# Kernel tuning notes

Measured on AMD Instinct MI355X. Metric: run time of the kernel, lower is better.

## Reference

```python
import jax, jax.numpy as jnp
import numpy as np

V, E, H, B, L = 128, 256, 4, 1024, 64
EPS5, EPS6 = 1e-5, 1e-6


def layer_norm(x, g, b, eps):
    m = x.mean(-1, keepdims=True)
    v = ((x - m) ** 2).mean(-1, keepdims=True)
    return (x - m) * jax.lax.rsqrt(v + eps) * g + b


def get_pos(max_len, emb_dim):
    # matches torch get_pos: freq[i] = 10000**(-i/half)
    half = emb_dim // 2
    freq = jnp.power(10000.0, -jnp.arange(half, dtype=jnp.float32) / half)
    phase = jnp.arange(max_len, dtype=jnp.float32)[:, None] * freq[None, :]
    pe = jnp.zeros((max_len, emb_dim), jnp.float32)
    pe = pe.at[:, 0::2].set(jnp.sin(phase)).at[:, 1::2].set(jnp.cos(phase))
    return pe


def setup_inputs() -> dict:
    key = jax.random.key(0)
    ks = jax.random.split(key, 8)
    char_code = jax.random.randint(ks[0], (B, L), 0, V)
    emb_table = (jax.random.normal(ks[1], (V, E), jnp.float32) * 0.02).at[0].set(0.0)  # padding_idx=0
    qkv_w = jax.random.normal(ks[2], (3 * E * H, E), jnp.float32) * 0.02
    fc_w = jax.random.normal(ks[3], (E, E * H), jnp.float32) * 0.02
    fc_b = jnp.zeros((E,), jnp.float32)
    ff_w1 = jax.random.normal(ks[4], (E, E), jnp.float32) * 0.02
    ff_b1 = jnp.zeros((E,), jnp.float32)
    ff_w2 = jax.random.normal(ks[5], (E, E), jnp.float32) * 0.02
    ff_b2 = jnp.zeros((E,), jnp.float32)
    ones = jnp.ones((E,), jnp.float32)
    zeros = jnp.zeros((E,), jnp.float32)
    return dict(char_code=char_code, max_len=L, emb_table=emb_table, qkv_w=qkv_w,
                ln0_g=ones, ln0_b=zeros, fc_w=fc_w, fc_b=fc_b,
                sln_g=ones, sln_b=zeros, ln1_g=ones, ln1_b=zeros,
                ff_w1=ff_w1, ff_b1=ff_b1, ff_w2=ff_w2, ff_b2=ff_b2,
                ffln_g=ones, ffln_b=zeros, ln2_g=ones, ln2_b=zeros)


def reference(char_code, max_len, emb_table, qkv_w, ln0_g, ln0_b, fc_w, fc_b,
              sln_g, sln_b, ln1_g, ln1_b, ff_w1, ff_b1, ff_w2, ff_b2,
              ffln_g, ffln_b, ln2_g, ln2_b):
    cc = char_code[:, :max_len]                      # [B,L]
    pos = get_pos(max_len, E)                        # [L,E]
    x = layer_norm(emb_table[cc] + pos[None], ln0_g, ln0_b, EPS5)  # [B,L,E]
    mask = (cc == 0)                                 # [B,L] key mask

    # scaled_dot_product_attention (eval mode, dropout inactive)
    x2 = x + pos[None]                               # pos added a second time (faithful)
    qkv = jnp.einsum('ble,fe->blf', x2, qkv_w)       # [B,L,3*E*H]
    qkv = qkv.reshape(B, max_len, H, 3 * E).transpose(0, 2, 1, 3)  # [B,H,L,3E]
    q, k, v = jnp.split(qkv, 3, axis=-1)             # each [B,H,L,E]
    qk = jnp.einsum('bhqe,bhke->bhqk', q, k) / (E ** 0.5)
    qk = jnp.where(mask[:, None, None, :], -jnp.inf, qk)
    attn = jax.nn.softmax(qk, axis=-1)               # [B,H,L,L]
    nm = (~mask).astype(jnp.float32)                 # [B,L]
    nw = nm.sum(-1)                                  # [B]
    score = jnp.einsum('bq,bhqk->bhk', nm, attn) / nw[:, None, None]  # [B,H,L]
    out = jnp.einsum('bhl,bhle->bhe', score, v)      # [B,H,E]
    out = out.reshape(B, H * E) @ fc_w.T + fc_b      # [B,E]
    out = layer_norm(out, sln_g, sln_b, EPS5)

    word = layer_norm(out + x.mean(1), ln1_g, ln1_b, EPS5)
    # FeedForward bug in source: returns layer_norm(x), ignoring x + layers(x)
    ff = layer_norm(word, ffln_g, ffln_b, EPS6)
    word = ff + word
    word = layer_norm(word, ln2_g, ln2_b, EPS5)
    return word
```

## Files before the change

### kernel.cpp

```cpp
#include <hip/hip_runtime.h>


typedef __attribute__((ext_vector_type(8))) short bf16x8;
typedef __attribute__((ext_vector_type(4))) float f32x4;

__device__ __forceinline__ float wred_sum(float v) {
#pragma unroll
  for (int off = 32; off > 0; off >>= 1) v += __shfl_xor(v, off, 64);
  return v;
}
__device__ __forceinline__ float bf2f(unsigned short u) {
  union { unsigned int i; float f; } x; x.i = ((unsigned int)u) << 16; return x.f;
}
__device__ __forceinline__ unsigned short f2bf(float f) {
  union { float f; unsigned int i; } x; x.f = f;
  unsigned int r = x.i + 0x7FFFu + ((x.i >> 16) & 1u);
  return (unsigned short)(r >> 16);
}
__device__ __forceinline__ void gld16(const unsigned short* g, unsigned short* l) {
  __builtin_amdgcn_global_load_lds(
      (const __attribute__((address_space(1))) unsigned int*)g,
      (__attribute__((address_space(3))) unsigned int*)l, 16, 0, 0);
}
__device__ __forceinline__ float fast_freq(float i) {
  return exp2f(i * (-13.287712379549449f / 128.0f));
}

__global__ __launch_bounds__(256) void prep_kernel(const float* qkv_w, const float* fc_w,
                                                   const float* emb, const float* ln0_g,
                                                   const float* ln0_b, float* posmean,
                                                   unsigned short* NTb, unsigned short* wfoldb,
                                                   unsigned short* x2tb) {
  __shared__ float T[64][65];
  __shared__ unsigned short As[64 * 64];
  __shared__ unsigned short Bs[64 * 64];
  int bid = blockIdx.x, t = threadIdx.x;

  if (bid < 128) {
    int w = t >> 6, lane = t & 63;
    int li = lane & 15, hi = lane >> 4;
    int r = t >> 4, c4 = (t & 15) * 4;
    bool isNT = bid < 64;
    int sub = isNT ? bid : bid - 64;
    int h = sub >> 4;
    int tm = (sub >> 2) & 3;
    int tn = sub & 3;
    int m0 = tm * 64, n0 = tn * 64;
    f32x4 acc[4] = {};
    for (int kt = 0; kt < 4; ++kt) {
      int k0 = kt * 64;
      if (isNT) {
        __syncthreads();
#pragma unroll
        for (int rep = 0; rep < 4; ++rep) {
          int il = rep * 16 + r;
          float4 v = *(const float4*)(qkv_w + (size_t)(h * 768 + 256 + k0 + il) * 256 + m0 + c4);
          T[il][c4] = v.x; T[il][c4 + 1] = v.y; T[il][c4 + 2] = v.z; T[il][c4 + 3] = v.w;
        }
        __syncthreads();
#pragma unroll
        for (int rep = 0; rep < 4; ++rep) {
          int el = rep * 16 + r;
          As[el * 64 + c4 + 0] = f2bf(T[c4 + 0][el]);
          As[el * 64 + c4 + 1] = f2bf(T[c4 + 1][el]);
          As[el * 64 + c4 + 2] = f2bf(T[c4 + 2][el]);
          As[el * 64 + c4 + 3] = f2bf(T[c4 + 3][el]);
        }
      } else {
        __syncthreads();
#pragma unroll
        for (int rep = 0; rep < 4; ++rep) {
          int rl = rep * 16 + r;
          float4 v = *(const float4*)(fc_w + (size_t)(m0 + rl) * 1024 + h * 256 + k0 + c4);
          As[rl * 64 + c4 + 0] = f2bf(v.x);
          As[rl * 64 + c4 + 1] = f2bf(v.y);
          As[rl * 64 + c4 + 2] = f2bf(v.z);
          As[rl * 64 + c4 + 3] = f2bf(v.w);
        }
      }
      {
        int sel = isNT ? 0 : 512;
        __syncthreads();
#pragma unroll
        for (int rep = 0; rep < 4; ++rep) {
          int il = rep * 16 + r;
          float4 v = *(const float4*)(qkv_w + (size_t)(h * 768 + sel + k0 + il) * 256 + n0 + c4);
          T[il][c4] = v.x; T[il][c4 + 1] = v.y; T[il][c4 + 2] = v.z; T[il][c4 + 3] = v.w;
        }
        __syncthreads();
#pragma unroll
        for (int rep = 0; rep < 4; ++rep) {
          int el = rep * 16 + r;
          Bs[el * 64 + c4 + 0] = f2bf(T[c4 + 0][el]);
          Bs[el * 64 + c4 + 1] = f2bf(T[c4 + 1][el]);
          Bs[el * 64 + c4 + 2] = f2bf(T[c4 + 2][el]);
          Bs[el * 64 + c4 + 3] = f2bf(T[c4 + 3][el]);
        }
      }
      __syncthreads();
#pragma unroll
      for (int kk = 0; kk < 2; ++kk) {
        bf16x8 bf = *(const bf16x8*)(Bs + (w * 16 + li) * 64 + kk * 32 + hi * 8);
#pragma unroll
        for (int m = 0; m < 4; ++m) {
          bf16x8 af = *(const bf16x8*)(As + (m * 16 + li) * 64 + kk * 32 + hi * 8);
          acc[m] = __builtin_amdgcn_mfma_f32_16x16x32_bf16(af, bf, acc[m], 0, 0, 0);
        }
      }
    }
    if (isNT) {
      unsigned short* C = NTb + (size_t)h * 65536;
      int col = n0 + w * 16 + li;
#pragma unroll
      for (int m = 0; m < 4; ++m)
#pragma unroll
        for (int j = 0; j < 4; ++j)
          C[(size_t)(m0 + m * 16 + hi * 4 + j) * 256 + col] = f2bf(acc[m][j]);
    } else {
      int col = h * 256 + n0 + w * 16 + li;
#pragma unroll
      for (int m = 0; m < 4; ++m)
#pragma unroll
        for (int j = 0; j < 4; ++j)
          wfoldb[(size_t)(m0 + m * 16 + hi * 4 + j) * 1024 + col] = f2bf(acc[m][j]);
    }
  } else if (bid == 128) {
    int e = t;
    float freq = fast_freq((float)(e >> 1));
    float s = 0.f;
    for (int l = 0; l < 64; ++l) {
      float ph = (float)l * freq;
      s += (e & 1) ? __cosf(ph) : __sinf(ph);
    }
    posmean[e] = s * (1.0f / 64.0f);
  } else {
    int w = t >> 6, lane = t & 63;
    int row = (bid - 129) * 4 + w;
    int c = row >> 6, l = row & 63;
    int e0 = lane * 4;
    float fr0 = fast_freq((float)(e0 >> 1));
    float fr1 = fast_freq((float)(e0 >> 1) + 1.0f);
    float p0 = (float)l * fr0, p1 = (float)l * fr1;
    float4 pv = make_float4(__sinf(p0), __cosf(p0), __sinf(p1), __cosf(p1));
    float4 ev = *(const float4*)(emb + c * 256 + e0);
    float v0 = ev.x + pv.x, v1 = ev.y + pv.y, v2 = ev.z + pv.z, v3 = ev.w + pv.w;
    float s = wred_sum(v0 + v1 + v2 + v3);
    float q = wred_sum(v0 * v0 + v1 * v1 + v2 * v2 + v3 * v3);
    float mean = s * (1.0f / 256.0f);
    float var = q * (1.0f / 256.0f) - mean * mean;
    float rstd = rsqrtf(var + 1e-5f);
    float4 gv = *(const float4*)(ln0_g + e0);
    float4 bv = *(const float4*)(ln0_b + e0);
    *(ushort4*)(x2tb + (size_t)row * 256 + e0) = make_ushort4(
        f2bf((v0 - mean) * rstd * gv.x + bv.x + pv.x),
        f2bf((v1 - mean) * rstd * gv.y + bv.y + pv.y),
        f2bf((v2 - mean) * rstd * gv.z + bv.z + pv.z),
        f2bf((v3 - mean) * rstd * gv.w + bv.w + pv.w));
  }
}

__global__ __launch_bounds__(256) void gemm128_kernel(const unsigned short* A,
                                                      const unsigned short* B,
                                                      unsigned short* C) {
  __shared__ unsigned short S[2 * 128 * 64];
  unsigned short* As = S;
  unsigned short* Bs = S + 128 * 64;
  int t = threadIdx.x, w = t >> 6, lane = t & 63;
  int m0 = blockIdx.y * 128, n0 = blockIdx.x * 128, z = blockIdx.z;
  B += (size_t)z * 65536;
  int wr = w >> 1, wc = w & 1;
  f32x4 acc[4][4] = {};
  int r_in = lane >> 3, cb = (lane & 7) * 8;
  for (int kt = 0; kt < 4; ++kt) {
#pragma unroll
    for (int it = 0; it < 4; ++it) {
      int rowblk = it * 32 + w * 8;
      gld16(A + (size_t)(m0 + rowblk + r_in) * 256 + kt * 64 + cb, As + rowblk * 64);
      gld16(B + (size_t)(n0 + rowblk + r_in) * 256 + kt * 64 + cb, Bs + rowblk * 64);
    }
    __syncthreads();
#pragma unroll
    for (int kk = 0; kk < 2; ++kk) {
      bf16x8 af[4], bfr[4];
#pragma unroll
      for (int m = 0; m < 4; ++m)
        af[m] = *(const bf16x8*)(As + (wr * 64 + m * 16 + (lane & 15)) * 64 + kk * 32 + (lane >> 4) * 8);
#pragma unroll
      for (int n = 0; n < 4; ++n)
        bfr[n] = *(const bf16x8*)(Bs + (wc * 64 + n * 16 + (lane & 15)) * 64 + kk * 32 + (lane >> 4) * 8);
#pragma unroll
      for (int m = 0; m < 4; ++m)
#pragma unroll
        for (int n = 0; n < 4; ++n)
          acc[m][n] = __builtin_amdgcn_mfma_f32_16x16x32_bf16(af[m], bfr[n], acc[m][n], 0, 0, 0);
    }
    __syncthreads();
  }
  unsigned short* Cs = S;
#pragma unroll
  for (int m = 0; m < 4; ++m)
#pragma unroll
    for (int n = 0; n < 4; ++n) {
      int row = wr * 64 + m * 16 + ((lane >> 4)) * 4;
      int col = wc * 64 + n * 16 + (lane & 15);
#pragma unroll
      for (int j = 0; j < 4; ++j)
        Cs[(row + j) * 128 + col] = f2bf(acc[m][n][j]);
    }
  __syncthreads();
#pragma unroll
  for (int it = 0; it < 8; ++it) {
    int row = it * 16 + (t >> 4);
    int ce = (t & 15) * 8;
    *(bf16x8*)(C + (size_t)(m0 + row) * 1024 + z * 256 + n0 + ce) =
        *(const bf16x8*)(Cs + row * 128 + ce);
  }
}

__global__ __launch_bounds__(512, 4) void attn_kernel(const int* cc, const unsigned short* yt,
                                                      const unsigned short* x2tb,
                                                      const float* posmean,
                                                      unsigned short* svb, float* xmb) {
  __shared__ unsigned short X2s[4 * 4112];
  __shared__ float s_sp[8][64];
  __shared__ float s_nm[64];
  __shared__ int s_cc[64];
  __shared__ float s_nwinv;
  int b = blockIdx.x;
  int t = threadIdx.x, w = t >> 6, lane = t & 63;
  int li = lane & 15, hi = lane >> 4;
  int h = w >> 1, mh = w & 1;

  if (t < 64) {
    int c = cc[b * 64 + t];
    s_cc[t] = c;
    s_nm[t] = (c != 0) ? 1.0f : 0.0f;
  }
  __syncthreads();
  if (t < 64) {
    float s = wred_sum(s_nm[t]);
    if (t == 0) s_nwinv = 1.0f / s;
  }

  int sr = lane >> 3;
  int sg = (lane & 7) ^ sr;
  {
    int idx = w * 8 + sr;
    size_t rbase = (size_t)(s_cc[idx] * 64 + idx) * 256;
#pragma unroll
    for (int ecc = 0; ecc < 4; ++ecc)
      gld16(x2tb + rbase + ecc * 64 + sg * 8, X2s + ecc * 4112 + w * 512);
  }

  const unsigned short* rowp[2];
#pragma unroll
  for (int m = 0; m < 2; ++m) {
    int idx = mh * 32 + m * 16 + li;
    rowp[m] = yt + (size_t)(s_cc[idx] * 64 + idx) * 1024 + h * 256;
  }
  float nmv[4];
#pragma unroll
  for (int n = 0; n < 4; ++n) nmv[n] = s_nm[n * 16 + li];

  bf16x8 ybuf[4][4];
#pragma unroll
  for (int ec = 0; ec < 2; ++ec)
#pragma unroll
    for (int kk = 0; kk < 2; ++kk)
#pragma unroll
      for (int m = 0; m < 2; ++m)
        ybuf[ec][kk * 2 + m] = *(const bf16x8*)(rowp[m] + ec * 64 + kk * 32 + hi * 8);

  __syncthreads();

  f32x4 acc[2][4] = {};
#pragma unroll
  for (int ec = 0; ec < 4; ++ec) {
    if (ec < 2) {
#pragma unroll
      for (int kk = 0; kk < 2; ++kk)
#pragma unroll
        for (int m = 0; m < 2; ++m)
          ybuf[ec + 2][kk * 2 + m] = *(const bf16x8*)(rowp[m] + (ec + 2) * 64 + kk * 32 + hi * 8);
    }
    __builtin_amdgcn_sched_barrier(0);
    __builtin_amdgcn_s_setprio(1);
#pragma unroll
    for (int kk = 0; kk < 2; ++kk)
#pragma unroll
      for (int n = 0; n < 4; ++n) {
        int rk = n * 16 + li;
        bf16x8 bf = *(const bf16x8*)(X2s + ec * 4112 + rk * 64 + (((kk * 4 + hi) ^ (rk & 7)) * 8));
#pragma unroll
        for (int m = 0; m < 2; ++m)
          acc[m][n] = __builtin_amdgcn_mfma_f32_16x16x32_bf16(ybuf[ec][kk * 2 + m], bf, acc[m][n], 0, 0, 0);
      }
    __builtin_amdgcn_s_setprio(0);
  }

  float sc[4] = {0.f, 0.f, 0.f, 0.f};
#pragma unroll
  for (int m = 0; m < 2; ++m)
#pragma unroll
    for (int j = 0; j < 4; ++j) {
      float nmq = s_nm[mh * 32 + m * 16 + hi * 4 + j];
      float p[4];
#pragma unroll
      for (int n = 0; n < 4; ++n) p[n] = nmv[n] * __expf(acc[m][n][j] * 0.0625f);
      float s = (p[0] + p[1]) + (p[2] + p[3]);
      s += __shfl_xor(s, 1, 64);
      s += __shfl_xor(s, 2, 64);
      s += __shfl_xor(s, 4, 64);
      s += __shfl_xor(s, 8, 64);
      float f = nmq / s;
#pragma unroll
      for (int n = 0; n < 4; ++n) sc[n] += p[n] * f;
    }
#pragma unroll
  for (int n = 0; n < 4; ++n) {
    sc[n] += __shfl_xor(sc[n], 16, 64);
    sc[n] += __shfl_xor(sc[n], 32, 64);
  }
  if (hi == 0) {
#pragma unroll
    for (int n = 0; n < 4; ++n) s_sp[w][n * 16 + li] = sc[n];
  }
  __syncthreads();

  {
    float nwinv = s_nwinv;
    int c0 = mh * 128 + lane * 2;
    int chunk = c0 >> 6;
    int cin = c0 & 63;
    int cg = cin >> 3, ce = cin & 7;
    const unsigned short* Xc = X2s + chunk * 4112;
    const float* spa = s_sp[h * 2];
    const float* spb = s_sp[h * 2 + 1];
    float o0 = 0.f, o1 = 0.f;
#pragma unroll
    for (int k = 0; k < 64; ++k) {
      float sk = (spa[k] + spb[k]) * nwinv;
      const unsigned short* p = Xc + k * 64 + ((cg ^ (k & 7)) * 8) + ce;
      o0 = fmaf(sk, bf2f(p[0]), o0);
      o1 = fmaf(sk, bf2f(p[1]), o1);
    }
    ushort2 ov; ov.x = f2bf(o0); ov.y = f2bf(o1);
    *(ushort2*)(svb + (size_t)b * 1024 + h * 256 + c0) = ov;
  }

  {
    int cidx = w * 32 + (lane & 31);
    int chunk = cidx >> 6, cin = cidx & 63;
    int cg = cin >> 3, ce = cin & 7;
    const unsigned short* Xc = X2s + chunk * 4112;
    int r0 = lane >> 5;
    float s = 0.f;
#pragma unroll
    for (int kk = 0; kk < 32; ++kk) {
      int k = r0 + kk * 2;
      s += bf2f(Xc[k * 64 + ((cg ^ (k & 7)) * 8) + ce]);
    }
    s += __shfl_xor(s, 32, 64);
    if (lane < 32)
      xmb[(size_t)b * 256 + cidx] = s * (1.0f / 64.0f) - posmean[cidx];
  }
}

__global__ __launch_bounds__(256) void fc_mfma_kernel(const unsigned short* aob,
                                                      const unsigned short* fc_wb,
                                                      float* fco) {
  __shared__ unsigned short As[64 * 64];
  __shared__ unsigned short Bs[64 * 64];
  int t = threadIdx.x, w = t >> 6, lane = t & 63;
  int li = lane & 15, hi = lane >> 4;
  int n0 = blockIdx.x * 64;
  int m0 = blockIdx.y * 64;
  int z = blockIdx.z;
  int r_in = lane >> 3, cb = (lane & 7) * 8;
  f32x4 acc[4] = {};
  for (int kt = z * 4; kt < z * 4 + 4; ++kt) {
#pragma unroll
    for (int it = 0; it < 2; ++it) {
      int rowblk = it * 32 + w * 8;
      gld16(aob + (size_t)(m0 + rowblk + r_in) * 1024 + kt * 64 + cb, As + rowblk * 64);
      gld16(fc_wb + (size_t)(n0 + rowblk + r_in) * 1024 + kt * 64 + cb, Bs + rowblk * 64);
    }
    __syncthreads();
#pragma unroll
    for (int kk = 0; kk < 2; ++kk) {
      bf16x8 bf = *(const bf16x8*)(Bs + (w * 16 + li) * 64 + kk * 32 + hi * 8);
#pragma unroll
      for (int m = 0; m < 4; ++m) {
        bf16x8 af = *(const bf16x8*)(As + (m * 16 + li) * 64 + kk * 32 + hi * 8);
        acc[m] = __builtin_amdgcn_mfma_f32_16x16x32_bf16(af, bf, acc[m], 0, 0, 0);
      }
    }
    __syncthreads();
  }
  int col = n0 + w * 16 + li;
  float* out = fco + (size_t)z * 262144;
#pragma unroll
  for (int m = 0; m < 4; ++m)
#pragma unroll
    for (int j = 0; j < 4; ++j)
      out[(size_t)(m0 + m * 16 + hi * 4 + j) * 256 + col] = acc[m][j];
}

__device__ __forceinline__ float block_ln(float v, int t, float eps, const float* g,
                                          const float* b, float* s_part) {
  int w = t >> 6, lane = t & 63;
  __syncthreads();
  float s = wred_sum(v), q = wred_sum(v * v);
  if (lane == 0) { s_part[w] = s; s_part[4 + w] = q; }
  __syncthreads();
  float sum = s_part[0] + s_part[1] + s_part[2] + s_part[3];
  float sq = s_part[4] + s_part[5] + s_part[6] + s_part[7];
  float mean = sum * (1.0f / 256.0f);
  float var = sq * (1.0f / 256.0f) - mean * mean;
  float rstd = rsqrtf(var + eps);
  return (v - mean) * rstd * g[t] + b[t];
}

__global__ __launch_bounds__(256) void final_kernel(
    const float* xmb, const float* fco, const float* fc_b,
    const float* sln_g, const float* sln_b, const float* ln1_g, const float* ln1_b,
    const float* ffln_g, const float* ffln_b, const float* ln2_g, const float* ln2_b,
    float* out) {
  __shared__ float s_part[8];
  int b = blockIdx.x, t = threadIdx.x;
  size_t o = (size_t)b * 256 + t;
  float xm = xmb[o];
  float v = fco[o] + fco[262144 + o] + fco[2 * 262144 + o] + fco[3 * 262144 + o] + fc_b[t];
  v = block_ln(v, t, 1e-5f, sln_g, sln_b, s_part);
  v = v + xm;
  v = block_ln(v, t, 1e-5f, ln1_g, ln1_b, s_part);
  float ff = block_ln(v, t, 1e-6f, ffln_g, ffln_b, s_part);
  float w2 = ff + v;
  float fin = block_ln(w2, t, 1e-5f, ln2_g, ln2_b, s_part);
  out[b * 256 + t] = fin;
}

extern "C" void kernel_launch(void* const* d_in, const int* in_sizes, int n_in,
                              void* d_out, int out_size, void* d_ws, size_t ws_size,
                              hipStream_t stream) {
  const int* char_code = (const int*)d_in[0];
  const float* emb    = (const float*)d_in[2];
  const float* qkv_w  = (const float*)d_in[3];
  const float* ln0_g  = (const float*)d_in[4];
  const float* ln0_b  = (const float*)d_in[5];
  const float* fc_w   = (const float*)d_in[6];
  const float* fc_b   = (const float*)d_in[7];
  const float* sln_g  = (const float*)d_in[8];
  const float* sln_b  = (const float*)d_in[9];
  const float* ln1_g  = (const float*)d_in[10];
  const float* ln1_b  = (const float*)d_in[11];
  const float* ffln_g = (const float*)d_in[16];
  const float* ffln_b = (const float*)d_in[17];
  const float* ln2_g  = (const float*)d_in[18];
  const float* ln2_b  = (const float*)d_in[19];

  float* ws = (float*)d_ws;
  float* posmean = ws;
  unsigned short* x2tb  = (unsigned short*)(posmean + 256);
  unsigned short* yt    = x2tb + (size_t)8192 * 256;
  unsigned short* NTb   = yt + (size_t)8192 * 1024;
  unsigned short* wfoldb= NTb + 262144;
  unsigned short* svb   = wfoldb + 262144;
  float* fco = (float*)(svb + (size_t)1024 * 1024);
  float* xmb = fco + (size_t)4 * 262144;

  prep_kernel<<<2177, 256, 0, stream>>>(qkv_w, fc_w, emb, ln0_g, ln0_b, posmean,
                                        NTb, wfoldb, x2tb);
  gemm128_kernel<<<dim3(2, 64, 4), 256, 0, stream>>>(x2tb, NTb, yt);
  attn_kernel<<<1024, 512, 0, stream>>>(char_code, yt, x2tb, posmean, svb, xmb);
  fc_mfma_kernel<<<dim3(4, 16, 4), 256, 0, stream>>>(svb, wfoldb, fco);
  final_kernel<<<1024, 256, 0, stream>>>(xmb, fco, fc_b,
                                         sln_g, sln_b, ln1_g, ln1_b,
                                         ffln_g, ffln_b, ln2_g, ln2_b, (float*)d_out);
}
```

Before: 65.63 us.

## Fuse fc GEMM with final layernorm chain and swizzle gemm128 block order

Merges the split-K fc GEMM and the final layernorm kernel into one kernel. Each 512-thread block computes 16 full output rows over all of K, holds them in LDS, and runs the four layernorms with wave-level reductions. This drops one launch, the fp32 partial-sum buffer round-trip and the block-wide syncs. It also remaps the gemm128 grid to a 1D swizzled block order so blocks that share operands run close together in time. In exchange, the fused kernel launches only 64 blocks, each looping over all 16 K tiles serially, so parallelism is far lower than before.

```diff
diff --git a/kernel.cpp b/kernel.cpp
--- a/kernel.cpp
+++ b/kernel.cpp
@@ -166,7 +166,10 @@
   unsigned short* As = S;
   unsigned short* Bs = S + 128 * 64;
   int t = threadIdx.x, w = t >> 6, lane = t & 63;
-  int m0 = blockIdx.y * 128, n0 = blockIdx.x * 128, z = blockIdx.z;
+  int bid = blockIdx.x;
+  int swz = (bid & 7) * 64 + (bid >> 3);
+  int xb = swz & 1, yb = (swz >> 1) & 63, z = swz >> 7;
+  int m0 = yb * 128, n0 = xb * 128;
   B += (size_t)z * 65536;
   int wr = w >> 1, wc = w & 1;
   f32x4 acc[4][4] = {};
@@ -366,78 +369,81 @@
   }
 }
 
-__global__ __launch_bounds__(256) void fc_mfma_kernel(const unsigned short* aob,
-                                                      const unsigned short* fc_wb,
-                                                      float* fco) {
-  __shared__ unsigned short As[64 * 64];
-  __shared__ unsigned short Bs[64 * 64];
-  int t = threadIdx.x, w = t >> 6, lane = t & 63;
-  int li = lane & 15, hi = lane >> 4;
-  int n0 = blockIdx.x * 64;
-  int m0 = blockIdx.y * 64;
-  int z = blockIdx.z;
-  int r_in = lane >> 3, cb = (lane & 7) * 8;
-  f32x4 acc[4] = {};
-  for (int kt = z * 4; kt < z * 4 + 4; ++kt) {
-#pragma unroll
-    for (int it = 0; it < 2; ++it) {
-      int rowblk = it * 32 + w * 8;
-      gld16(aob + (size_t)(m0 + rowblk + r_in) * 1024 + kt * 64 + cb, As + rowblk * 64);
-      gld16(fc_wb + (size_t)(n0 + rowblk + r_in) * 1024 + kt * 64 + cb, Bs + rowblk * 64);
-    }
-    __syncthreads();
-#pragma unroll
-    for (int kk = 0; kk < 2; ++kk) {
-      bf16x8 bf = *(const bf16x8*)(Bs + (w * 16 + li) * 64 + kk * 32 + hi * 8);
-#pragma unroll
-      for (int m = 0; m < 4; ++m) {
-        bf16x8 af = *(const bf16x8*)(As + (m * 16 + li) * 64 + kk * 32 + hi * 8);
-        acc[m] = __builtin_amdgcn_mfma_f32_16x16x32_bf16(af, bf, acc[m], 0, 0, 0);
-      }
-    }
-    __syncthreads();
-  }
-  int col = n0 + w * 16 + li;
-  float* out = fco + (size_t)z * 262144;
-#pragma unroll
-  for (int m = 0; m < 4; ++m)
-#pragma unroll
-    for (int j = 0; j < 4; ++j)
-      out[(size_t)(m0 + m * 16 + hi * 4 + j) * 256 + col] = acc[m][j];
-}
-
-__device__ __forceinline__ float block_ln(float v, int t, float eps, const float* g,
-                                          const float* b, float* s_part) {
-  int w = t >> 6, lane = t & 63;
-  __syncthreads();
-  float s = wred_sum(v), q = wred_sum(v * v);
-  if (lane == 0) { s_part[w] = s; s_part[4 + w] = q; }
-  __syncthreads();
-  float sum = s_part[0] + s_part[1] + s_part[2] + s_part[3];
-  float sq = s_part[4] + s_part[5] + s_part[6] + s_part[7];
-  float mean = sum * (1.0f / 256.0f);
-  float var = sq * (1.0f / 256.0f) - mean * mean;
+__device__ __forceinline__ float4 ln4(float4 v, const float* g, const float* b, int e0,
+                                      float eps) {
+  float s = wred_sum(v.x + v.y + v.z + v.w);
+  float q = wred_sum(v.x * v.x + v.y * v.y + v.z * v.z + v.w * v.w);
+  float mean = s * (1.0f / 256.0f);
+  float var = q * (1.0f / 256.0f) - mean * mean;
   float rstd = rsqrtf(var + eps);
-  return (v - mean) * rstd * g[t] + b[t];
-}
-
-__global__ __launch_bounds__(256) void final_kernel(
-    const float* xmb, const float* fco, const float* fc_b,
+  float4 g4 = *(const float4*)(g + e0);
+  float4 b4 = *(const float4*)(b + e0);
+  return make_float4((v.x - mean) * rstd * g4.x + b4.x,
+                     (v.y - mean) * rstd * g4.y + b4.y,
+                     (v.z - mean) * rstd * g4.z + b4.z,
+                     (v.w - mean) * rstd * g4.w + b4.w);
+}
+
+__global__ __launch_bounds__(512) void fcfin_kernel(
+    const unsigned short* svbp, const unsigned short* wfoldb, const float* fc_b,
+    const float* xmb,
     const float* sln_g, const float* sln_b, const float* ln1_g, const float* ln1_b,
     const float* ffln_g, const float* ffln_b, const float* ln2_g, const float* ln2_b,
     float* out) {
-  __shared__ float s_part[8];
-  int b = blockIdx.x, t = threadIdx.x;
-  size_t o = (size_t)b * 256 + t;
-  float xm = xmb[o];
-  float v = fco[o] + fco[262144 + o] + fco[2 * 262144 + o] + fco[3 * 262144 + o] + fc_b[t];
-  v = block_ln(v, t, 1e-5f, sln_g, sln_b, s_part);
-  v = v + xm;
-  v = block_ln(v, t, 1e-5f, ln1_g, ln1_b, s_part);
-  float ff = block_ln(v, t, 1e-6f, ffln_g, ffln_b, s_part);
-  float w2 = ff + v;
-  float fin = block_ln(w2, t, 1e-5f, ln2_g, ln2_b, s_part);
-  out[b * 256 + t] = fin;
+  __shared__ unsigned short As[16 * 64];
+  __shared__ unsigned short Bs[256 * 64];
+  __shared__ float Outs[16 * 256];
+  int t = threadIdx.x, w = t >> 6, lane = t & 63;
+  int li = lane & 15, hi = lane >> 4;
+  int m0 = blockIdx.x * 16;
+  int sr = lane >> 3, sg = lane & 7;
+  f32x4 acc[2] = {};
+  for (int kt = 0; kt < 16; ++kt) {
+    if (w < 2) {
+      int row = w * 8 + sr;
+      gld16(svbp + (size_t)(m0 + row) * 1024 + kt * 64 + sg * 8, As + w * 512);
+    }
+#pragma unroll
+    for (int it = 0; it < 4; ++it) {
+      int rowblk = it * 64 + w * 8;
+      gld16(wfoldb + (size_t)(rowblk + sr) * 1024 + kt * 64 + sg * 8, Bs + rowblk * 64);
+    }
+    __syncthreads();
+#pragma unroll
+    for (int kk = 0; kk < 2; ++kk) {
+      bf16x8 af = *(const bf16x8*)(As + li * 64 + kk * 32 + hi * 8);
+#pragma unroll
+      for (int nn = 0; nn < 2; ++nn) {
+        bf16x8 bf = *(const bf16x8*)(Bs + (w * 32 + nn * 16 + li) * 64 + kk * 32 + hi * 8);
+        acc[nn] = __builtin_amdgcn_mfma_f32_16x16x32_bf16(af, bf, acc[nn], 0, 0, 0);
+      }
+    }
+    __syncthreads();
+  }
+#pragma unroll
+  for (int nn = 0; nn < 2; ++nn)
+#pragma unroll
+    for (int j = 0; j < 4; ++j)
+      Outs[(hi * 4 + j) * 256 + w * 32 + nn * 16 + li] = acc[nn][j];
+  __syncthreads();
+
+  int e0 = lane * 4;
+  float4 bias = *(const float4*)(fc_b + e0);
+#pragma unroll
+  for (int bb = 0; bb < 2; ++bb) {
+    int row = w * 2 + bb;
+    int gb = m0 + row;
+    float4 v = *(const float4*)(Outs + row * 256 + e0);
+    v.x += bias.x; v.y += bias.y; v.z += bias.z; v.w += bias.w;
+    v = ln4(v, sln_g, sln_b, e0, 1e-5f);
+    float4 xm = *(const float4*)(xmb + (size_t)gb * 256 + e0);
+    v.x += xm.x; v.y += xm.y; v.z += xm.z; v.w += xm.w;
+    v = ln4(v, ln1_g, ln1_b, e0, 1e-5f);
+    float4 ff = ln4(v, ffln_g, ffln_b, e0, 1e-6f);
+    float4 w2 = make_float4(v.x + ff.x, v.y + ff.y, v.z + ff.z, v.w + ff.w);
+    float4 fin = ln4(w2, ln2_g, ln2_b, e0, 1e-5f);
+    *(float4*)(out + (size_t)gb * 256 + e0) = fin;
+  }
 }
 
 extern "C" void kernel_launch(void* const* d_in, const int* in_sizes, int n_in,
@@ -466,15 +472,13 @@
   unsigned short* NTb   = yt + (size_t)8192 * 1024;
   unsigned short* wfoldb= NTb + 262144;
   unsigned short* svb   = wfoldb + 262144;
-  float* fco = (float*)(svb + (size_t)1024 * 1024);
-  float* xmb = fco + (size_t)4 * 262144;
+  float* xmb = (float*)(svb + (size_t)1024 * 1024);
 
   prep_kernel<<<2177, 256, 0, stream>>>(qkv_w, fc_w, emb, ln0_g, ln0_b, posmean,
                                         NTb, wfoldb, x2tb);
-  gemm128_kernel<<<dim3(2, 64, 4), 256, 0, stream>>>(x2tb, NTb, yt);
+  gemm128_kernel<<<512, 256, 0, stream>>>(x2tb, NTb, yt);
   attn_kernel<<<1024, 512, 0, stream>>>(char_code, yt, x2tb, posmean, svb, xmb);
-  fc_mfma_kernel<<<dim3(4, 16, 4), 256, 0, stream>>>(svb, wfoldb, fco);
-  final_kernel<<<1024, 256, 0, stream>>>(xmb, fco, fc_b,
-                                         sln_g, sln_b, ln1_g, ln1_b,
-                                         ffln_g, ffln_b, ln2_g, ln2_b, (float*)d_out);
-}
+  fcfin_kernel<<<64, 512, 0, stream>>>(svb, wfoldb, fc_b, xmb,
+                                       sln_g, sln_b, ln1_g, ln1_b,
+                                       ffln_g, ffln_b, ln2_g, ln2_b, (float*)d_out);
+}
```

New measurement: 74.92 us. 14.2% more time.
